# Kernel tuning notes

Measured on AMD Instinct MI355X. Metric: run time of the kernel, lower is better.

The kernel has to match this reference:

```python
import jax, jax.numpy as jnp
import numpy as np

IN, OUT, LR = 4096, 4096, 64
TILE = (8, 8)

def setup_inputs() -> dict:
    key = jax.random.key(0)
    ks = jax.random.split(key, 8)
    return {
        "x": jax.random.normal(ks[0], (4, 2048, IN), dtype=jnp.float32),
        "frozen_random_matrix": jax.random.normal(ks[1], (OUT, IN), dtype=jnp.float16),
        "lowrank_first": jax.random.normal(ks[2], (LR, IN), dtype=jnp.float32) * 0.02,
        "lowrank_second": jax.random.normal(ks[3], (2 * OUT, LR), dtype=jnp.float32) * 0.02,
        "grid_scale": jax.random.normal(ks[4], (OUT // TILE[0], 1, IN // TILE[1], 1), dtype=jnp.float32),
        "grid_bias": jax.random.normal(ks[5], (OUT // TILE[0], 1, IN // TILE[1], 1), dtype=jnp.float32),
        "sparse_adapter": jnp.zeros((OUT, IN), dtype=jnp.float32),
        "scale": jax.random.normal(ks[6], (OUT,), dtype=jnp.float32),
        "bias": jax.random.normal(ks[7], (OUT,), dtype=jnp.float32),
    }

def reference(x, frozen_random_matrix, lowrank_first, lowrank_second,
              grid_scale, grid_bias, sparse_adapter, scale, bias):
    O, I = frozen_random_matrix.shape
    th, tw = TILE
    # Tiled affine reconstruction of the weight matrix, in fp16 (buffer dtype)
    m = frozen_random_matrix.reshape(O // th, th, I // tw, tw)
    m = grid_bias.astype(jnp.float16) + m * grid_scale.astype(jnp.float16)
    m = m.reshape(O, I) + sparse_adapter.astype(jnp.float16)
    # Dense GEMM in fp16, cast back to input dtype (mirrors input.to(matrix.dtype))
    baseline = jnp.matmul(x.astype(jnp.float16), m.T).astype(x.dtype)  # [B,S,O]
    # Low-rank adapter path
    hid = jnp.matmul(x, lowrank_first.T)                               # [B,S,LR]
    intercept = jnp.concatenate([scale, bias], axis=0)                 # [2*O]
    proj = jnp.matmul(hid, lowrank_second.T) + intercept               # [B,S,2*O]
    multiplicative, additive = proj[..., :O], proj[..., O:]
    return additive + multiplicative * baseline
```

## Files before the change

### kernel.cpp

```cpp
#include <hip/hip_runtime.h>
#include <stdint.h>

typedef _Float16 f16;
typedef unsigned short u16;
typedef __attribute__((ext_vector_type(8))) _Float16 h16x8;
typedef __attribute__((ext_vector_type(8))) unsigned short u16x8;
typedef __attribute__((ext_vector_type(4))) float f32x4;

#define NDIM  4096
#define KDIM  4096
#define LRDIM 64
#define NTK   128

#define MFMA16(a, b, c) __builtin_amdgcn_mfma_f32_16x16x32_f16((a), (b), (c), 0, 0, 0)

__device__ __forceinline__ float bf2f(u16 b) {
  union { unsigned u; float f; } c; c.u = ((unsigned)b) << 16; return c.f;
}
__device__ __forceinline__ float h2f(u16 b) {
  union { u16 u; f16 h; } c; c.u = b; return (float)c.h;
}
__device__ __forceinline__ h16x8 pack8(float4 a, float4 b) {
  h16x8 w = { (f16)a.x, (f16)a.y, (f16)a.z, (f16)a.w,
              (f16)b.x, (f16)b.y, (f16)b.z, (f16)b.w };
  return w;
}

__device__ __forceinline__ void gll16(const void* g, void* l) {
  __builtin_amdgcn_global_load_lds(
      (const __attribute__((address_space(1))) void*)g,
      (__attribute__((address_space(3))) void*)l,
      16, 0, 0);
}

__device__ int frozen_mode(const void* frozen, int t) {
  const u16* fr = (const u16*)frozen;
  __shared__ int sE[256], sO[256];
  int ce = 0, co = 0;
  for (int j = 0; j < 8; ++j) {
    float ve = fabsf(bf2f(fr[t * 16 + 2 * j]));
    float vo = fabsf(bf2f(fr[t * 16 + 2 * j + 1]));
    if (ve >= 0.05f && ve <= 10.0f) ++ce;
    if (vo >= 0.05f && vo <= 10.0f) ++co;
  }
  sE[t] = ce; sO[t] = co;
  __syncthreads();
  for (int s = 128; s > 0; s >>= 1) {
    if (t < s) { sE[t] += sE[t + s]; sO[t] += sO[t + s]; }
    __syncthreads();
  }
  int te = sE[0], to = sO[0];
  __syncthreads();
  if (to > 1024) return (te > 1024) ? 1 : 2;
  return 0;
}

__device__ __forceinline__ h16x8 build_m8(
    const void* __restrict__ frozen, const float* __restrict__ gs,
    const float* __restrict__ gb, const float* __restrict__ sa,
    int o, int i0, int mode)
{
  size_t fo = (size_t)o * KDIM + i0;
  int gidx = (o >> 3) * 512 + (i0 >> 3);
  float gsf = gs[gidx], gbf = gb[gidx];
  float4 s0 = ((const float4*)(sa + fo))[0];
  float4 s1 = ((const float4*)(sa + fo))[1];
  float sv[8] = { s0.x, s0.y, s0.z, s0.w, s1.x, s1.y, s1.z, s1.w };
  float fv[8];
  if (mode == 2) {
    float4 q0 = ((const float4*)((const float*)frozen + fo))[0];
    float4 q1 = ((const float4*)((const float*)frozen + fo))[1];
    fv[0]=q0.x; fv[1]=q0.y; fv[2]=q0.z; fv[3]=q0.w;
    fv[4]=q1.x; fv[5]=q1.y; fv[6]=q1.z; fv[7]=q1.w;
  } else {
    u16x8 fb = *(const u16x8*)((const u16*)frozen + fo);
#pragma unroll
    for (int j = 0; j < 8; ++j) fv[j] = (mode == 1) ? bf2f(fb[j]) : h2f(fb[j]);
  }
  h16x8 w;
#pragma unroll
  for (int j = 0; j < 8; ++j) w[j] = (f16)(gbf + fv[j] * gsf + sv[j]);
  return w;
}

__global__ __launch_bounds__(256) void k9_build_m(
    const void* __restrict__ frozen, const float* __restrict__ gs,
    const float* __restrict__ gb, const float* __restrict__ sa,
    f16* __restrict__ mW)
{
  int mode = frozen_mode(frozen, threadIdx.x);
  int idx = blockIdx.x * 256 + threadIdx.x;
  int o  = idx >> 9;
  int ig = idx & 511;
  h16x8 w = build_m8(frozen, gs, gb, sa, o, ig * 8, mode);
  *(h16x8*)(mW + (size_t)o * KDIM + ig * 8) = w;
}

__global__ __launch_bounds__(256) void k9_cast_x(const float* __restrict__ x,
                                                 f16* __restrict__ xh)
{
  size_t idx = (size_t)blockIdx.x * 256 + threadIdx.x;
  const float4* xp = (const float4*)x + idx * 2;
  *(h16x8*)(xh + idx * 8) = pack8(xp[0], xp[1]);
}

__global__ __launch_bounds__(256) void k14_hid(const f16* __restrict__ xh,
                                               const float* __restrict__ L1,
                                               f16* __restrict__ hid)
{
  __shared__ f16 sA[2][32 * 32];
  __shared__ f16 sB[2][64 * 32];
  int t = threadIdx.x;
  int l = t & 63, wid = t >> 6;
  int wr = wid >> 1, wc = wid & 1;
  int brow = blockIdx.x * 32;
  int ar = t >> 2, ac8 = (t & 3) * 8;
  int brw = t >> 2, bc8 = (t & 3) * 8;

  f32x4 acc[2] = {};

  {
    if (t < 128)
      gll16(xh + (size_t)(brow + ar) * KDIM + ac8, &sA[0][ar * 32 + ac8]);
    const float* lp = L1 + (size_t)brw * KDIM + bc8;
    *(h16x8*)&sB[0][brw * 32 + bc8] = pack8(((const float4*)lp)[0], ((const float4*)lp)[1]);
  }

  int cur = 0;
  const int NT = KDIM / 32;
  for (int kt = 0; kt < NT; ++kt) {
    __syncthreads();
    bool pf = (kt + 1 < NT);
    h16x8 wb;
    if (pf) {
      int k0 = (kt + 1) * 32;
      if (t < 128)
        gll16(xh + (size_t)(brow + ar) * KDIM + k0 + ac8, &sA[cur ^ 1][ar * 32 + ac8]);
      const float* lp = L1 + (size_t)brw * KDIM + k0 + bc8;
      wb = pack8(((const float4*)lp)[0], ((const float4*)lp)[1]);
    }
    h16x8 aF, bF[2];
    aF = *(const h16x8*)&sA[cur][(wr * 16 + (l & 15)) * 32 + (l >> 4) * 8];
#pragma unroll
    for (int n = 0; n < 2; ++n)
      bF[n] = *(const h16x8*)&sB[cur][(wc * 32 + n * 16 + (l & 15)) * 32 + (l >> 4) * 8];
#pragma unroll
    for (int n = 0; n < 2; ++n)
      acc[n] = MFMA16(aF, bF[n], acc[n]);
    if (pf)
      *(h16x8*)&sB[cur ^ 1][brw * 32 + bc8] = wb;
    cur ^= 1;
  }

#pragma unroll
  for (int n = 0; n < 2; ++n)
#pragma unroll
    for (int j = 0; j < 4; ++j) {
      int r = wr * 16 + ((l >> 4) << 2) + j;
      int c = wc * 32 + n * 16 + (l & 15);
      hid[(size_t)(brow + r) * LRDIM + c] = (f16)acc[n][j];
    }
}

__global__ __launch_bounds__(512) void k18b_main(
    const f16* __restrict__ xh, const f16* __restrict__ mW,
    const f16* __restrict__ hid, const float* __restrict__ L2,
    const float* __restrict__ scale, const float* __restrict__ bias,
    float* __restrict__ out)
{
  __shared__ f16 lds[3][16384];

  int t = threadIdx.x;
  int l = t & 63, wid = t >> 6;
  int wm = wid >> 2, wn = wid & 3;

  int wg = blockIdx.x;
  int xcd = wg & 7, w = wg >> 3;
  int bm = xcd * 4 + (w & 3);
  int bn = w >> 2;
  int brow = bm * 256, bcol = bn * 256;

  auto stage = [&](int q, int kt2, int buf) {
    int u = q * 512 + t;
    if (u < 1024) {
      int sg = (u & 3) ^ ((u >> 3) & 3);
      gll16(xh + (size_t)(brow + (u >> 2)) * KDIM + kt2 * 32 + sg * 8,
            &lds[buf][u * 8]);
    } else {
      int v = u - 1024;
      int sg = (v & 3) ^ ((v >> 3) & 3);
      gll16(mW + (size_t)(bcol + (v >> 2)) * KDIM + kt2 * 32 + sg * 8,
            &lds[buf][8192 + v * 8]);
    }
  };

#pragma unroll
  for (int q = 0; q < 4; ++q) stage(q, 0, 0);
#pragma unroll
  for (int q = 0; q < 4; ++q) stage(q, 1, 1);
  asm volatile("s_waitcnt vmcnt(4)" ::: "memory");
  __builtin_amdgcn_sched_barrier(0);
  __builtin_amdgcn_s_barrier();

  f32x4 acc[8][4] = {};

  int X = ((l >> 4) ^ ((l >> 1) & 3)) * 8;

  for (int kt = 0; kt < NTK; ++kt) {
    const f16* A = &lds[kt % 3][0];
    const f16* B = &lds[kt % 3][8192];
    int sb = (kt + 2) % 3;
    bool st = (kt + 2) < NTK;
    int k2 = kt + 2;

    int ar0 = (wm * 128 + (l & 15)) * 32 + X;
    int br0 = (wn * 64  + (l & 15)) * 32 + X;

    h16x8 aF[4], bF[4];

#pragma unroll
    for (int f = 0; f < 4; ++f) aF[f] = *(const h16x8*)&A[ar0 + f * 512];
    bF[0] = *(const h16x8*)&B[br0];
    bF[1] = *(const h16x8*)&B[br0 + 512];
    if (st) stage(0, k2, sb);
    __builtin_amdgcn_s_barrier();
    __builtin_amdgcn_s_setprio(1);
#pragma unroll
    for (int f = 0; f < 4; ++f) {
      acc[f][0] = MFMA16(aF[f], bF[0], acc[f][0]);
      acc[f][1] = MFMA16(aF[f], bF[1], acc[f][1]);
    }
    __builtin_amdgcn_s_setprio(0);
    __builtin_amdgcn_s_barrier();

    bF[2] = *(const h16x8*)&B[br0 + 1024];
    bF[3] = *(const h16x8*)&B[br0 + 1536];
    if (st) stage(1, k2, sb);
    __builtin_amdgcn_s_barrier();
    __builtin_amdgcn_s_setprio(1);
#pragma unroll
    for (int f = 0; f < 4; ++f) {
      acc[f][2] = MFMA16(aF[f], bF[2], acc[f][2]);
      acc[f][3] = MFMA16(aF[f], bF[3], acc[f][3]);
    }
    __builtin_amdgcn_s_setprio(0);
    __builtin_amdgcn_s_barrier();

#pragma unroll
    for (int f = 0; f < 4; ++f) aF[f] = *(const h16x8*)&A[ar0 + (f + 4) * 512];
    if (st) stage(2, k2, sb);
    __builtin_amdgcn_s_barrier();
    __builtin_amdgcn_s_setprio(1);
#pragma unroll
    for (int f = 0; f < 4; ++f) {
      acc[f + 4][0] = MFMA16(aF[f], bF[0], acc[f + 4][0]);
      acc[f + 4][1] = MFMA16(aF[f], bF[1], acc[f + 4][1]);
    }
    __builtin_amdgcn_s_setprio(0);
    __builtin_amdgcn_s_barrier();

    if (st) stage(3, k2, sb);
    if (kt < NTK - 2) {
      asm volatile("s_waitcnt vmcnt(4)" ::: "memory");
    } else {
      asm volatile("s_waitcnt vmcnt(0)" ::: "memory");
    }
    __builtin_amdgcn_sched_barrier(0);
    __builtin_amdgcn_s_barrier();
    __builtin_amdgcn_s_setprio(1);
#pragma unroll
    for (int f = 0; f < 4; ++f) {
      acc[f + 4][2] = MFMA16(aF[f], bF[2], acc[f + 4][2]);
      acc[f + 4][3] = MFMA16(aF[f], bF[3], acc[f + 4][3]);
    }
    __builtin_amdgcn_s_setprio(0);
    __builtin_amdgcn_s_barrier();
  }

  f16* sH  = &lds[0][0];
  f16* sLm = &lds[1][0];
  f16* sLa = &lds[2][0];

#pragma unroll
  for (int q = 0; q < 4; ++q) {
    int u = q * 512 + t;
    gll16(hid + (size_t)(brow + (u >> 3)) * LRDIM + (u & 7) * 8, &sH[u * 8]);
  }
#pragma unroll
  for (int q = 0; q < 4; ++q) {
    int u = q * 512 + t;
    const float* lp = L2 + (size_t)(bcol + (u >> 3)) * LRDIM + (u & 7) * 8;
    *(h16x8*)&sLm[u * 8] = pack8(((const float4*)lp)[0], ((const float4*)lp)[1]);
  }
#pragma unroll
  for (int q = 0; q < 4; ++q) {
    int u = q * 512 + t;
    const float* lp = L2 + (size_t)(NDIM + bcol + (u >> 3)) * LRDIM + (u & 7) * 8;
    *(h16x8*)&sLa[u * 8] = pack8(((const float4*)lp)[0], ((const float4*)lp)[1]);
  }
  __syncthreads();

  float sc[4], bi[4];
#pragma unroll
  for (int n = 0; n < 4; ++n) {
    int o = bcol + wn * 64 + n * 16 + (l & 15);
    sc[n] = scale[o];
    bi[n] = bias[o];
  }

  {
    h16x8 lB[4][2];
#pragma unroll
    for (int n = 0; n < 4; ++n)
#pragma unroll
      for (int kk = 0; kk < 2; ++kk)
        lB[n][kk] = *(const h16x8*)&sLm[(wn * 64 + n * 16 + (l & 15)) * 64 + kk * 32 + (l >> 4) * 8];
#pragma unroll
    for (int f = 0; f < 8; ++f) {
      h16x8 h0 = *(const h16x8*)&sH[(wm * 128 + f * 16 + (l & 15)) * 64 + (l >> 4) * 8];
      h16x8 h1 = *(const h16x8*)&sH[(wm * 128 + f * 16 + (l & 15)) * 64 + 32 + (l >> 4) * 8];
      f32x4 mm[4];
#pragma unroll
      for (int n = 0; n < 4; ++n) {
        f32x4 mi = { sc[n], sc[n], sc[n], sc[n] };
        mm[n] = mi;
      }
#pragma unroll
      for (int n = 0; n < 4; ++n) {
        mm[n] = MFMA16(h0, lB[n][0], mm[n]);
        mm[n] = MFMA16(h1, lB[n][1], mm[n]);
      }
#pragma unroll
      for (int n = 0; n < 4; ++n)
        acc[f][n] *= mm[n];
    }
  }

  {
    h16x8 lB[4][2];
#pragma unroll
    for (int n = 0; n < 4; ++n)
#pragma unroll
      for (int kk = 0; kk < 2; ++kk)
        lB[n][kk] = *(const h16x8*)&sLa[(wn * 64 + n * 16 + (l & 15)) * 64 + kk * 32 + (l >> 4) * 8];
#pragma unroll
    for (int f = 0; f < 8; ++f) {
      h16x8 h0 = *(const h16x8*)&sH[(wm * 128 + f * 16 + (l & 15)) * 64 + (l >> 4) * 8];
      h16x8 h1 = *(const h16x8*)&sH[(wm * 128 + f * 16 + (l & 15)) * 64 + 32 + (l >> 4) * 8];
      f32x4 aa[4];
#pragma unroll
      for (int n = 0; n < 4; ++n) {
        f32x4 mi = { bi[n], bi[n], bi[n], bi[n] };
        aa[n] = mi;
      }
#pragma unroll
      for (int n = 0; n < 4; ++n) {
        aa[n] = MFMA16(h0, lB[n][0], aa[n]);
        aa[n] = MFMA16(h1, lB[n][1], aa[n]);
      }
      int rbase = brow + wm * 128 + f * 16 + ((l >> 4) << 2);
#pragma unroll
      for (int n = 0; n < 4; ++n) {
        int c = bcol + wn * 64 + n * 16 + (l & 15);
        f32x4 v = aa[n] + acc[f][n];
#pragma unroll
        for (int j = 0; j < 4; ++j)
          out[(size_t)(rbase + j) * NDIM + c] = v[j];
      }
    }
  }
}

extern "C" void kernel_launch(void* const* d_in, const int* in_sizes, int n_in,
                              void* d_out, int out_size, void* d_ws, size_t ws_size,
                              hipStream_t stream)
{
  const int SD[9] = {33554432,16777216,262144,524288,262144,262144,16777216,4096,4096};
  const int SA[9] = {4096,16777216,262144,262144,262144,524288,4096,16777216,33554432};
  bool dict = (n_in == 9), alph = (n_in == 9);
  if (n_in == 9) {
    for (int i = 0; i < 9; ++i) {
      if (in_sizes[i] != SD[i]) dict = false;
      if (in_sizes[i] != SA[i]) alph = false;
    }
  }
  if (!dict && !alph) {
    int ix = 0;
    for (int i = 0; i < n_in; ++i)
      if (in_sizes[i] == 33554432 || in_sizes[i] == 134217728) { ix = i; break; }
    dict = (ix == 0);
  }
  const float* x     = (const float*)d_in[dict ? 0 : 8];
  const void*  fr    =               d_in[1];
  const float* L1    = (const float*)d_in[dict ? 2 : 4];
  const float* L2    = (const float*)d_in[dict ? 3 : 5];
  const float* gs    = (const float*)d_in[dict ? 4 : 3];
  const float* gb    = (const float*)d_in[dict ? 5 : 2];
  const float* sa    = (const float*)d_in[dict ? 6 : 7];
  const float* scale = (const float*)d_in[dict ? 7 : 6];
  const float* bias  = (const float*)d_in[dict ? 8 : 0];
  float* out = (float*)d_out;

  const size_t MW_B = (size_t)NDIM * KDIM * 2;
  const size_t XH_B = (size_t)8192 * KDIM * 2;

  char* ws = (char*)d_ws;
  f16* mW  = (f16*)ws;
  f16* xh  = (f16*)(ws + MW_B);
  f16* hid = (f16*)(ws + MW_B + XH_B);

  k9_cast_x<<<dim3(16384), dim3(256), 0, stream>>>(x, xh);
  k9_build_m<<<dim3(8192), dim3(256), 0, stream>>>(fr, gs, gb, sa, mW);
  k14_hid<<<dim3(256), dim3(256), 0, stream>>>(xh, L1, hid);
  k18b_main<<<dim3(512), dim3(512), 0, stream>>>(
      xh, mW, hid, L2, scale, bias, out);
}
```

Baseline: 425.4 us.

## Merge prep kernels and simplify main GEMM loop to one barrier phase

Two changes. The x-cast and weight-build kernels are merged into one launch so a kernel boundary and its tail go away. The main GEMM loop drops its four-phase interleaving of LDS reads, staging and MFMA, where each phase had its own barriers and priority toggles. Instead each iteration issues all four stage loads for tile kt+2 up front, waits with vmcnt(8) so two tiles can be in flight, and then runs all 32 MFMAs in one block. This removes many per-iteration barriers but loses the fine-grained overlap of LDS fragment loads with MFMA, and holding all eight A fragments raises register pressure.

```diff
diff --git a/kernel.cpp b/kernel.cpp
--- a/kernel.cpp
+++ b/kernel.cpp
@@ -83,25 +83,25 @@
   return w;
 }
 
-__global__ __launch_bounds__(256) void k9_build_m(
-    const void* __restrict__ frozen, const float* __restrict__ gs,
-    const float* __restrict__ gb, const float* __restrict__ sa,
+__global__ __launch_bounds__(256) void k_prep(
+    const float* __restrict__ x, const void* __restrict__ frozen,
+    const float* __restrict__ gs, const float* __restrict__ gb,
+    const float* __restrict__ sa, f16* __restrict__ xh,
     f16* __restrict__ mW)
 {
-  int mode = frozen_mode(frozen, threadIdx.x);
-  int idx = blockIdx.x * 256 + threadIdx.x;
-  int o  = idx >> 9;
-  int ig = idx & 511;
-  h16x8 w = build_m8(frozen, gs, gb, sa, o, ig * 8, mode);
-  *(h16x8*)(mW + (size_t)o * KDIM + ig * 8) = w;
-}
-
-__global__ __launch_bounds__(256) void k9_cast_x(const float* __restrict__ x,
-                                                 f16* __restrict__ xh)
-{
-  size_t idx = (size_t)blockIdx.x * 256 + threadIdx.x;
-  const float4* xp = (const float4*)x + idx * 2;
-  *(h16x8*)(xh + idx * 8) = pack8(xp[0], xp[1]);
+  int b = blockIdx.x;
+  if (b < 16384) {
+    size_t idx = (size_t)b * 256 + threadIdx.x;
+    const float4* xp = (const float4*)x + idx * 2;
+    *(h16x8*)(xh + idx * 8) = pack8(xp[0], xp[1]);
+  } else {
+    int mode = frozen_mode(frozen, threadIdx.x);
+    int idx = (b - 16384) * 256 + threadIdx.x;
+    int o  = idx >> 9;
+    int ig = idx & 511;
+    h16x8 w = build_m8(frozen, gs, gb, sa, o, ig * 8, mode);
+    *(h16x8*)(mW + (size_t)o * KDIM + ig * 8) = w;
+  }
 }
 
 __global__ __launch_bounds__(256) void k14_hid(const f16* __restrict__ xh,
@@ -162,7 +162,7 @@
     }
 }
 
-__global__ __launch_bounds__(512) void k18b_main(
+__global__ __launch_bounds__(512) void k18c_main(
     const f16* __restrict__ xh, const f16* __restrict__ mW,
     const f16* __restrict__ hid, const float* __restrict__ L2,
     const float* __restrict__ scale, const float* __restrict__ bias,
@@ -198,9 +198,6 @@
   for (int q = 0; q < 4; ++q) stage(q, 0, 0);
 #pragma unroll
   for (int q = 0; q < 4; ++q) stage(q, 1, 1);
-  asm volatile("s_waitcnt vmcnt(4)" ::: "memory");
-  __builtin_amdgcn_sched_barrier(0);
-  __builtin_amdgcn_s_barrier();
 
   f32x4 acc[8][4] = {};
 
@@ -210,70 +207,39 @@
     const f16* A = &lds[kt % 3][0];
     const f16* B = &lds[kt % 3][8192];
     int sb = (kt + 2) % 3;
-    bool st = (kt + 2) < NTK;
-    int k2 = kt + 2;
-
-    int ar0 = (wm * 128 + (l & 15)) * 32 + X;
-    int br0 = (wn * 64  + (l & 15)) * 32 + X;
-
-    h16x8 aF[4], bF[4];
-
-#pragma unroll
-    for (int f = 0; f < 4; ++f) aF[f] = *(const h16x8*)&A[ar0 + f * 512];
-    bF[0] = *(const h16x8*)&B[br0];
-    bF[1] = *(const h16x8*)&B[br0 + 512];
-    if (st) stage(0, k2, sb);
-    __builtin_amdgcn_s_barrier();
-    __builtin_amdgcn_s_setprio(1);
-#pragma unroll
-    for (int f = 0; f < 4; ++f) {
-      acc[f][0] = MFMA16(aF[f], bF[0], acc[f][0]);
-      acc[f][1] = MFMA16(aF[f], bF[1], acc[f][1]);
-    }
-    __builtin_amdgcn_s_setprio(0);
-    __builtin_amdgcn_s_barrier();
-
-    bF[2] = *(const h16x8*)&B[br0 + 1024];
-    bF[3] = *(const h16x8*)&B[br0 + 1536];
-    if (st) stage(1, k2, sb);
-    __builtin_amdgcn_s_barrier();
-    __builtin_amdgcn_s_setprio(1);
-#pragma unroll
-    for (int f = 0; f < 4; ++f) {
-      acc[f][2] = MFMA16(aF[f], bF[2], acc[f][2]);
-      acc[f][3] = MFMA16(aF[f], bF[3], acc[f][3]);
-    }
-    __builtin_amdgcn_s_setprio(0);
-    __builtin_amdgcn_s_barrier();
-
-#pragma unroll
-    for (int f = 0; f < 4; ++f) aF[f] = *(const h16x8*)&A[ar0 + (f + 4) * 512];
-    if (st) stage(2, k2, sb);
-    __builtin_amdgcn_s_barrier();
-    __builtin_amdgcn_s_setprio(1);
-#pragma unroll
-    for (int f = 0; f < 4; ++f) {
-      acc[f + 4][0] = MFMA16(aF[f], bF[0], acc[f + 4][0]);
-      acc[f + 4][1] = MFMA16(aF[f], bF[1], acc[f + 4][1]);
-    }
-    __builtin_amdgcn_s_setprio(0);
-    __builtin_amdgcn_s_barrier();
-
-    if (st) stage(3, k2, sb);
+
+    if (kt + 2 < NTK) {
+#pragma unroll
+      for (int q = 0; q < 4; ++q) stage(q, kt + 2, sb);
+    }
+
     if (kt < NTK - 2) {
+      asm volatile("s_waitcnt vmcnt(8)" ::: "memory");
+    } else if (kt == NTK - 2) {
       asm volatile("s_waitcnt vmcnt(4)" ::: "memory");
     } else {
       asm volatile("s_waitcnt vmcnt(0)" ::: "memory");
     }
     __builtin_amdgcn_sched_barrier(0);
     __builtin_amdgcn_s_barrier();
+
+    int ar0 = (wm * 128 + (l & 15)) * 32 + X;
+    int br0 = (wn * 64  + (l & 15)) * 32 + X;
+
+    h16x8 aF[8], bF[4];
+#pragma unroll
+    for (int f = 0; f < 8; ++f) aF[f] = *(const h16x8*)&A[ar0 + f * 512];
+#pragma unroll
+    for (int n = 0; n < 4; ++n) bF[n] = *(const h16x8*)&B[br0 + n * 512];
+
     __builtin_amdgcn_s_setprio(1);
 #pragma unroll
-    for (int f = 0; f < 4; ++f) {
-      acc[f + 4][2] = MFMA16(aF[f], bF[2], acc[f + 4][2]);
-      acc[f + 4][3] = MFMA16(aF[f], bF[3], acc[f + 4][3]);
-    }
+    for (int f = 0; f < 8; ++f)
+#pragma unroll
+      for (int n = 0; n < 4; ++n)
+        acc[f][n] = MFMA16(aF[f], bF[n], acc[f][n]);
     __builtin_amdgcn_s_setprio(0);
+
     __builtin_amdgcn_s_barrier();
   }
 
@@ -409,9 +375,8 @@
   f16* xh  = (f16*)(ws + MW_B);
   f16* hid = (f16*)(ws + MW_B + XH_B);
 
-  k9_cast_x<<<dim3(16384), dim3(256), 0, stream>>>(x, xh);
-  k9_build_m<<<dim3(8192), dim3(256), 0, stream>>>(fr, gs, gb, sa, mW);
+  k_prep<<<dim3(24576), dim3(256), 0, stream>>>(x, fr, gs, gb, sa, xh, mW);
   k14_hid<<<dim3(256), dim3(256), 0, stream>>>(xh, L1, hid);
-  k18b_main<<<dim3(512), dim3(512), 0, stream>>>(
+  k18c_main<<<dim3(512), dim3(512), 0, stream>>>(
       xh, mW, hid, L2, scale, bias, out);
 }
```

Measured after the change: 420.6 us. About the same (-1.1%).
